# Kernel tuning notes

Measured on AMD Instinct MI355X. Metric: run time of the kernel, lower is better.

## Reference

```python
import jax, jax.numpy as jnp
import numpy as np
from jax import lax

B, TX, RX, RATE, DIMZ, HID, DIRS = 8192, 32, 32, 2, 64, 128, 2
S, FEAT = 2 * TX, 2 * TX + 1
BN_EPS = 1e-5
GD_STEP = 1e-6   # hardcoded in original forward
GD_ITERS = 10    # hardcoded in original forward


def setup_inputs() -> dict:
    key = jax.random.key(0)
    ks = jax.random.split(key, 9)
    sc = 1.0 / np.sqrt(HID)
    return {
        "y": jax.random.normal(ks[0], (B, 2 * RX), jnp.float32),
        "H": jax.random.normal(ks[1], (B, 2 * RX, 2 * TX), jnp.float32),
        "x_raw": jax.random.randint(ks[2], (B, 2 * TX, 1), 0, 2 ** RATE).astype(jnp.float32),
        "gru_w_ih": jax.random.uniform(ks[3], (DIRS, 3 * HID, FEAT), jnp.float32, -sc, sc),
        "gru_w_hh": jax.random.uniform(ks[4], (DIRS, 3 * HID, HID), jnp.float32, -sc, sc),
        "gru_b_ih": jax.random.uniform(ks[5], (DIRS, 3 * HID), jnp.float32, -sc, sc),
        "gru_b_hh": jax.random.uniform(ks[6], (DIRS, 3 * HID), jnp.float32, -sc, sc),
        "w_Wz": jax.random.normal(ks[7], (DIMZ, DIRS * HID), jnp.float32),
        "w_Wx": jax.random.normal(ks[8], (DIMZ, DIRS * HID), jnp.float32),
        "bn_gamma": jnp.ones((2 * TX,), jnp.float32),
        "bn_beta": jnp.zeros((2 * TX,), jnp.float32),
        "step_size": 1,
        "iterations": 10,
    }


def _gru_dir(x_seq, wih, whh, bih, bhh):
    # x_seq: (S, B, F); PyTorch GRU cell equations
    xg = jnp.einsum('sbf,gf->sbg', x_seq, wih) + bih  # (S, B, 3H)

    def step(h, xg_t):
        hg = h @ whh.T + bhh
        xr, xz, xn = jnp.split(xg_t, 3, axis=-1)
        hr, hz, hn = jnp.split(hg, 3, axis=-1)
        r = jax.nn.sigmoid(xr + hr)
        z = jax.nn.sigmoid(xz + hz)
        n = jnp.tanh(xn + r * hn)
        h = (1.0 - z) * n + z * h
        return h, h

    h0 = jnp.zeros((x_seq.shape[1], whh.shape[1]), x_seq.dtype)
    _, out = lax.scan(step, h0, xg)
    return out  # (S, B, H)


def reference(y, H, x_raw, gru_w_ih, gru_w_hh, gru_b_ih, gru_b_hh,
              w_Wz, w_Wx, bn_gamma, bn_beta, step_size, iterations):
    # Hty: (B, 2tx, 1), HtH: (B, 2tx, 2tx)
    Hty = jnp.einsum('brt,br->bt', H, y)[..., None]
    HtH = jnp.einsum('brt,bru->btu', H, H)

    # BatchNorm1d over channel dim 2tx (stats over batch and last dim)
    feats = jnp.concatenate([HtH, Hty], axis=-1)  # (B, 2tx, 2tx+1)
    mu = feats.mean(axis=(0, 2), keepdims=True)
    var = feats.var(axis=(0, 2), keepdims=True)
    feats = (feats - mu) / jnp.sqrt(var + BN_EPS)
    feats = feats * bn_gamma[None, :, None] + bn_beta[None, :, None]

    # bidirectional GRU over seq dim (seq_len = 2tx)
    x_seq = jnp.transpose(feats, (1, 0, 2))  # (S, B, F)
    fwd = _gru_dir(x_seq, gru_w_ih[0], gru_w_hh[0], gru_b_ih[0], gru_b_hh[0])
    bwd = _gru_dir(x_seq[::-1], gru_w_ih[1], gru_w_hh[1], gru_b_ih[1], gru_b_hh[1])[::-1]
    go = jnp.concatenate([fwd, bwd], axis=-1)  # (S, B, 2H)

    w_z = jnp.transpose(go @ w_Wz.T, (1, 2, 0))  # (B, dim_z, S)
    w_x = jnp.transpose(go @ w_Wx.T, (1, 0, 2))  # (B, S, dim_z)

    x_hat0 = 2.0 * x_raw - (2.0 ** RATE) + 1.0  # QAM symbols
    z0 = w_z @ x_hat0  # (B, dim_z, 1)

    # gradient-descent loop (step_size/iterations args ignored, as in source)
    wxt = jnp.swapaxes(w_x, 1, 2)        # (B, dim_z, 2tx)
    wxt_hty = wxt @ Hty                  # (B, dim_z, 1)
    whhw = wxt @ (HtH @ w_x)             # (B, dim_z, dim_z)
    two_step = 2.0 * GD_STEP

    def gd(zh, _):
        return zh + two_step * (wxt_hty - whhw @ zh), None

    z_hat, _ = lax.scan(gd, z0, None, length=GD_ITERS)
    return w_x @ z_hat  # (B, 2tx, 1)
```

## Files before the change

kernel.cpp:

```cpp
#include <hip/hip_runtime.h>
#include <math.h>


typedef __attribute__((ext_vector_type(8))) short s8v;
typedef __attribute__((ext_vector_type(4))) float f4v;

__device__ __forceinline__ short f2bf(float x) {
  unsigned u = __float_as_uint(x);
  u += 0x7fffu + ((u >> 16) & 1u);
  return (short)(u >> 16);
}
__device__ __forceinline__ float bf2f(short h) {
  return __uint_as_float(((unsigned)(unsigned short)h) << 16);
}
__device__ __forceinline__ void fma4(float4& c, float a, const float4 w) {
  c.x += a*w.x; c.y += a*w.y; c.z += a*w.z; c.w += a*w.w;
}
__device__ __forceinline__ float vget(const float4& v, int i) { return ((const float*)&v)[i]; }

#define MFMA(A, B, C) __builtin_amdgcn_mfma_f32_16x16x32_bf16((A), (B), (C), 0, 0, 0)

__global__ __launch_bounds__(256) void k_feats(
    const float* __restrict__ Hm, const float* __restrict__ y,
    short* __restrict__ fragX, float* __restrict__ htyU, float* __restrict__ bnacc)
{
  __shared__ __align__(16) float Hl[64][68];
  __shared__ float yl[64];
  __shared__ float s1[64], s2[64];
  const int b = blockIdx.x;
  const int tid = threadIdx.x;
  const float* Hb = Hm + (size_t)b*4096;
  for (int i = tid; i < 4096; i += 256) Hl[i>>6][i&63] = Hb[i];
  if (tid < 64) { yl[tid] = y[b*64+tid]; s1[tid] = 0.f; s2[tid] = 0.f; }
  __syncthreads();

  if (tid < 64) {
    float acc = 0.f;
    for (int r = 0; r < 64; ++r) acc += Hl[r][tid]*yl[r];
    htyU[tid*8192 + b] = acc;
    atomicAdd(&s1[tid], acc);
    atomicAdd(&s2[tid], acc*acc);
  }
  const int tg = tid & 15, ug = tid >> 4;
  float4 acc4[4];
  acc4[0]=acc4[1]=acc4[2]=acc4[3]=make_float4(0.f,0.f,0.f,0.f);
  for (int r = 0; r < 64; ++r) {
    const float4 tv = *(const float4*)&Hl[r][4*tg];
    const float4 uv = *(const float4*)&Hl[r][4*ug];
    #pragma unroll
    for (int tt=0;tt<4;++tt) fma4(acc4[tt], vget(tv,tt), uv);
  }
  const int mt   = (b >> 4) & 3;
  const int brow = b & 15;
  const int u0   = 4*ug;
  short* fbase = fragX + (size_t)(b >> 6)*64*8192
               + (mt*2 + (u0 >> 5))*512 + (brow + 16*((u0 >> 3) & 3))*8 + (u0 & 7);
  #pragma unroll
  for (int tt=0;tt<4;++tt) {
    const int t = 4*tg+tt;
    float sv=0.f, sq=0.f;
    short hib[4], lob[4];
    #pragma unroll
    for (int uu=0;uu<4;++uu) {
      const float v = vget(acc4[tt],uu);
      const short hi = f2bf(v);
      hib[uu] = hi; lob[uu] = f2bf(v - bf2f(hi));
      sv += v; sq += v*v;
    }
    short* dst = fbase + (size_t)t*8192;
    *(short4*)dst          = make_short4(hib[0],hib[1],hib[2],hib[3]);
    *(short4*)(dst + 4096) = make_short4(lob[0],lob[1],lob[2],lob[3]);
    sv += __shfl_down(sv,32); sq += __shfl_down(sq,32);
    sv += __shfl_down(sv,16); sq += __shfl_down(sq,16);
    if ((tid & 63) < 16) { atomicAdd(&s1[t], sv); atomicAdd(&s2[t], sq); }
  }
  __syncthreads();
  if (tid < 64) {
    atomicAdd(&bnacc[tid*16],      s1[tid]);
    atomicAdd(&bnacc[(64+tid)*16], s2[tid]);
  }
}

__global__ void k_bnfin(const float* __restrict__ bnacc, const float* __restrict__ gam,
                        const float* __restrict__ bet, float* __restrict__ bnac)
{
  const int t = threadIdx.x;
  if (t < 64) {
    const float inv = 1.f/532480.f;
    const float mu  = bnacc[t*16]*inv;
    const float var = bnacc[(64+t)*16]*inv - mu*mu;
    const float a = gam[t]*rsqrtf(var + 1e-5f);
    bnac[t] = a;
    bnac[64+t] = bet[t] - mu*a;
  }
}

__global__ __launch_bounds__(256) void k_prep(
    const float* __restrict__ wih, const float* __restrict__ whh,
    const float* __restrict__ Wz, const float* __restrict__ Wx,
    short* __restrict__ Wg, short* __restrict__ W2g, float* __restrict__ rowsum)
{
  const int i = blockIdx.x*256 + threadIdx.x;
  if (i < 294912) {
    const int dd = i / 147456, r = i % 147456;
    const int sp = r / 73728, r2 = r % 73728;
    const int chunk = r2 / 512, e = r2 % 512;
    const int lane = e >> 3, ii = e & 7;
    const int nt = chunk / 6, kt = chunk % 6;
    const int n = nt*16 + (lane & 15);
    const int k = kt*32 + (lane >> 4)*8 + ii;
    const float v = (k < 64) ? wih[dd*24960 + n*65 + k]
                             : whh[dd*49152 + n*128 + (k - 64)];
    const short hi = f2bf(v);
    Wg[i] = sp ? f2bf(v - bf2f(hi)) : hi;
  } else if (i < 360448) {
    const int t = i - 294912;
    const int dd = t / 32768, r = t % 32768;
    const int sp = r / 16384, r2 = r % 16384;
    const int chunk = r2 / 512, e = r2 % 512;
    const int lane = e >> 3, ii = e & 7;
    const int nt2 = chunk / 4, kt = chunk % 4;
    const int n2 = nt2*16 + (lane & 15);
    const int k = kt*32 + (lane >> 4)*8 + ii;
    const float v = (n2 < 64) ? Wx[n2*256 + dd*128 + k]
                              : Wz[(n2 - 64)*256 + dd*128 + k];
    const short hi = f2bf(v);
    W2g[t] = sp ? f2bf(v - bf2f(hi)) : hi;
  } else if (i < 361216) {
    const int t = i - 360448;
    const int dd = t / 384, g = t % 384;
    float ssum = 0.f;
    for (int f = 0; f < 65; ++f) ssum += wih[dd*24960 + g*65 + f];
    rowsum[t] = ssum;
  }
}

__global__ __launch_bounds__(512, 2) void k_scan(
    const short* __restrict__ fragX, const float* __restrict__ htyU,
    const float* __restrict__ xraw,
    const short* __restrict__ Wg, const short* __restrict__ W2g,
    const float* __restrict__ bih, const float* __restrict__ bhh,
    const float* __restrict__ rowsum, const float* __restrict__ bnac,
    const float* __restrict__ wih,
    float* __restrict__ wx_out, float* __restrict__ z0_out)
{
  __shared__ __align__(16) short Axb[16384];
  __shared__ __align__(16) short Ahb[32768];
  __shared__ __align__(16) float xl[64][68];
  __shared__ __align__(16) float htyl[64][68];
  __shared__ float bna[128];

  const int tid = threadIdx.x;
  const int l   = tid & 63;
  const int w   = __builtin_amdgcn_readfirstlane(tid >> 6);
  const int tile = blockIdx.x >> 1, d = blockIdx.x & 1;
  const int b0  = tile * 64;
  const int l15 = l & 15, lq = l >> 4;
  const int j   = 16*w + l15;

  const short* Wgd = Wg  + d*147456;
  const short* W2d = W2g + d*32768;
  float* wxo = wx_out + (size_t)d * (8192ull*4096ull);
  float* z0o = z0_out + (size_t)d * (8192ull*64ull);

  s8v BR[6][2], BZ[6][2], BN[6][2], BP[4][2];
  #pragma unroll
  for (int kt = 0; kt < 6; ++kt)
    #pragma unroll
    for (int sp = 0; sp < 2; ++sp) {
      BR[kt][sp] = *(const s8v*)&Wgd[((sp*24 + w     )*6 + kt)*512 + l*8];
      BZ[kt][sp] = *(const s8v*)&Wgd[((sp*24 + 8 + w )*6 + kt)*512 + l*8];
      BN[kt][sp] = *(const s8v*)&Wgd[((sp*24 + 16 + w)*6 + kt)*512 + l*8];
    }
  #pragma unroll
  for (int kt = 0; kt < 4; ++kt)
    #pragma unroll
    for (int sp = 0; sp < 2; ++sp)
      BP[kt][sp] = *(const s8v*)&W2d[((sp*8 + w)*4 + kt)*512 + l*8];

  const float rsR = rowsum[d*384 + j];
  const float rsZ = rowsum[d*384 + 128 + j];
  const float rsN = rowsum[d*384 + 256 + j];
  const float KR  = bih[d*384 + j]       + bhh[d*384 + j];
  const float KZ  = bih[d*384 + 128 + j] + bhh[d*384 + 128 + j];
  const float KN  = bih[d*384 + 256 + j];
  const float BHN = bhh[d*384 + 256 + j];
  const float w64r = wih[d*24960 + j*65 + 64];
  const float w64z = wih[d*24960 + (128 + j)*65 + 64];
  const float w64n = wih[d*24960 + (256 + j)*65 + 64];

  const int hw_base = (j >> 5)*512 + ((j >> 3) & 3)*128 + (j & 7);

  for (int i = tid; i < 32768; i += 512) Ahb[i] = 0;
  for (int i = tid; i < 4096; i += 512) {
    const int bl = i >> 6, s = i & 63;
    xl[s][bl] = 2.f*xraw[(size_t)(b0 + bl)*64 + s] - 3.f;
  }
  for (int i = tid; i < 4096; i += 512) {
    const int s = i >> 6, bl = i & 63;
    htyl[s][bl] = htyU[s*8192 + b0 + bl];
  }
  if (tid < 128) bna[tid] = bnac[tid];

  f4v hprev[4], z0a[4];
  #pragma unroll
  for (int mt = 0; mt < 4; ++mt) { hprev[mt] = (f4v)0.f; z0a[mt] = (f4v)0.f; }

  {
    const int s0 = d ? 63 : 0;
    const short* src = fragX + (size_t)(tile*64 + s0)*8192;
    *(float4*)((char*)Axb + tid*16)        = *(const float4*)((const char*)src + tid*16);
    *(float4*)((char*)Axb + 8192 + tid*16) = *(const float4*)((const char*)src + 8192 + tid*16);
  }
  __syncthreads();

  for (int it = 0; it < 64; ++it) {
    const int s  = d ? 63 - it : it;
    const int sn = (it < 63) ? (d ? s - 1 : s + 1) : s;

    short* AxR = Axb + ((it & 1) << 13);
    short* AxW = Axb + (((it + 1) & 1) << 13);
    short* AhR = Ahb + (((it + 1) & 1) << 14);
    short* AhW = Ahb + ((it & 1) << 14);

    const short* srcn = fragX + (size_t)(tile*64 + sn)*8192;
    const float4 pf0 = *(const float4*)((const char*)srcn + tid*16);
    const float4 pf1 = *(const float4*)((const char*)srcn + 8192 + tid*16);

    const float a_s = bna[s], c_s = bna[64 + s];
    const float crK = c_s*rsR + KR;
    const float czK = c_s*rsZ + KZ;
    const float cnK = c_s*rsN + KN;

    #pragma unroll
    for (int mt = 0; mt < 4; ++mt) {
      f4v Crx = (f4v)0.f, Czx = (f4v)0.f, Cnx = (f4v)0.f;
      f4v Crh = (f4v)0.f, Czh = (f4v)0.f, Cnh = (f4v)0.f;
      #pragma unroll
      for (int kt = 0; kt < 2; ++kt) {
        const s8v axh = *(const s8v*)&AxR[mt*1024 + kt*512 + l*8];
        const s8v axl = *(const s8v*)&AxR[4096 + mt*1024 + kt*512 + l*8];
        Crx = MFMA(axh, BR[kt][0], Crx); Crx = MFMA(axh, BR[kt][1], Crx); Crx = MFMA(axl, BR[kt][0], Crx);
        Czx = MFMA(axh, BZ[kt][0], Czx); Czx = MFMA(axh, BZ[kt][1], Czx); Czx = MFMA(axl, BZ[kt][0], Czx);
        Cnx = MFMA(axh, BN[kt][0], Cnx); Cnx = MFMA(axh, BN[kt][1], Cnx); Cnx = MFMA(axl, BN[kt][0], Cnx);
      }
      #pragma unroll
      for (int kh = 0; kh < 4; ++kh) {
        const s8v ahh = *(const s8v*)&AhR[mt*2048 + kh*512 + l*8];
        const s8v ahl = *(const s8v*)&AhR[8192 + mt*2048 + kh*512 + l*8];
        const int kt = 2 + kh;
        Crh = MFMA(ahh, BR[kt][0], Crh); Crh = MFMA(ahh, BR[kt][1], Crh); Crh = MFMA(ahl, BR[kt][0], Crh);
        Czh = MFMA(ahh, BZ[kt][0], Czh); Czh = MFMA(ahh, BZ[kt][1], Czh); Czh = MFMA(ahl, BZ[kt][0], Czh);
        Cnh = MFMA(ahh, BN[kt][0], Cnh); Cnh = MFMA(ahh, BN[kt][1], Cnh); Cnh = MFMA(ahl, BN[kt][0], Cnh);
      }
      const float4 av4 = *(const float4*)&htyl[s][mt*16 + lq*4];
      f4v av; av[0]=av4.x; av[1]=av4.y; av[2]=av4.z; av[3]=av4.w;
      Crx += av * w64r; Czx += av * w64z; Cnx += av * w64n;
      #pragma unroll
      for (int e = 0; e < 4; ++e) {
        const float rr  = 1.f/(1.f + __expf(-(a_s*Crx[e] + Crh[e] + crK)));
        const float zz  = 1.f/(1.f + __expf(-(a_s*Czx[e] + Czh[e] + czK)));
        const float pre = a_s*Cnx[e] + cnK + rr*(Cnh[e] + BHN);
        const float ax2 = fabsf(pre);
        const float ee  = __expf(-2.f*ax2);
        const float nn  = copysignf((1.f - ee)/(1.f + ee), pre);
        hprev[mt][e] = (1.f - zz)*nn + zz*hprev[mt][e];
      }
    }

    #pragma unroll
    for (int mt = 0; mt < 4; ++mt)
      #pragma unroll
      for (int e = 0; e < 4; ++e) {
        const float hv = hprev[mt][e];
        const short hi = f2bf(hv);
        const int ad = mt*2048 + hw_base + (lq*4 + e)*8;
        AhW[ad] = hi;
        AhW[8192 + ad] = f2bf(hv - bf2f(hi));
      }
    *(float4*)((char*)AxW + tid*16)        = pf0;
    *(float4*)((char*)AxW + 8192 + tid*16) = pf1;
    __syncthreads();

    #pragma unroll
    for (int mt = 0; mt < 4; ++mt) {
      f4v Cp = (f4v)0.f;
      #pragma unroll
      for (int kt = 0; kt < 4; ++kt) {
        const s8v ahh = *(const s8v*)&AhW[mt*2048 + kt*512 + l*8];
        const s8v ahl = *(const s8v*)&AhW[8192 + mt*2048 + kt*512 + l*8];
        Cp = MFMA(ahh, BP[kt][0], Cp);
        Cp = MFMA(ahh, BP[kt][1], Cp);
        Cp = MFMA(ahl, BP[kt][0], Cp);
      }
      if (w < 4) {
        #pragma unroll
        for (int e = 0; e < 4; ++e)
          wxo[(size_t)(b0 + mt*16 + lq*4 + e)*4096 + s*64 + 16*w + l15] = Cp[e];
      } else {
        const float4 xh4 = *(const float4*)&xl[s][mt*16 + lq*4];
        f4v xh; xh[0]=xh4.x; xh[1]=xh4.y; xh[2]=xh4.z; xh[3]=xh4.w;
        z0a[mt] += xh * Cp;
      }
    }
  }
  if (w >= 4) {
    #pragma unroll
    for (int mt = 0; mt < 4; ++mt)
      #pragma unroll
      for (int e = 0; e < 4; ++e)
        z0o[(size_t)(b0 + mt*16 + lq*4 + e)*64 + 16*(w-4) + l15] = z0a[mt][e];
  }
}

__global__ __launch_bounds__(256) void k_gd(
    const float* __restrict__ Hm, const float* __restrict__ y,
    const float* __restrict__ wxf, const float* __restrict__ wxb,
    const float* __restrict__ z0f, const float* __restrict__ z0b,
    float* __restrict__ out)
{
  __shared__ __align__(16) float Hl[64][68];
  __shared__ __align__(16) float wx[64][68];
  __shared__ __align__(16) float tmp[64][68];
  __shared__ float yl[64], wh[64], zv[64];
  const int b = blockIdx.x;
  const int tid = threadIdx.x;
  const float* Hb = Hm + (size_t)b*4096;
  for (int i = tid; i < 4096; i += 256) {
    Hl[i>>6][i&63] = Hb[i];
    wx[i>>6][i&63] = wxf[(size_t)b*4096 + i] + wxb[(size_t)b*4096 + i];
  }
  if (tid < 64) {
    yl[tid] = y[b*64+tid];
    zv[tid] = z0f[(size_t)b*64+tid] + z0b[(size_t)b*64+tid];
  }
  __syncthreads();
  const int zq = tid & 15, tq = tid >> 4;
  #pragma unroll
  for (int rr = 0; rr < 4; ++rr) {
    const int r = 4*tq + rr;
    float4 a = make_float4(0.f,0.f,0.f,0.f);
    for (int t = 0; t < 64; ++t) fma4(a, Hl[r][t], *(const float4*)&wx[t][4*zq]);
    *(float4*)&tmp[r][4*zq] = a;
  }
  __syncthreads();
  float (*ww)[68] = Hl;
  #pragma unroll
  for (int ii = 0; ii < 4; ++ii) {
    const int zi = 4*tq + ii;
    float4 a = make_float4(0.f,0.f,0.f,0.f);
    for (int r = 0; r < 64; ++r) fma4(a, tmp[r][zi], *(const float4*)&tmp[r][4*zq]);
    *(float4*)&ww[zi][4*zq] = a;
  }
  if (tid < 64) {
    float acc = 0.f;
    for (int r = 0; r < 64; ++r) acc += tmp[r][tid]*yl[r];
    wh[tid] = acc;
  }
  __syncthreads();
  for (int itr = 0; itr < 10; ++itr) {
    float nz = 0.f;
    if (tid < 64) {
      float mv = 0.f;
      for (int k2 = 0; k2 < 64; ++k2) mv += ww[tid][k2]*zv[k2];
      nz = zv[tid] + 2e-6f*(wh[tid] - mv);
    }
    __syncthreads();
    if (tid < 64) zv[tid] = nz;
    __syncthreads();
  }
  if (tid < 64) {
    float o = 0.f;
    for (int z2 = 0; z2 < 64; ++z2) o += wx[tid][z2]*zv[z2];
    out[(size_t)b*64 + tid] = o;
  }
}

extern "C" void kernel_launch(void* const* d_in, const int* in_sizes, int n_in,
                              void* d_out, int out_size, void* d_ws, size_t ws_size,
                              hipStream_t stream)
{
  const float* y    = (const float*)d_in[0];
  const float* Hm   = (const float*)d_in[1];
  const float* xraw = (const float*)d_in[2];
  const float* wih  = (const float*)d_in[3];
  const float* whh  = (const float*)d_in[4];
  const float* bih  = (const float*)d_in[5];
  const float* bhh  = (const float*)d_in[6];
  const float* Wz   = (const float*)d_in[7];
  const float* Wx   = (const float*)d_in[8];
  const float* gam  = (const float*)d_in[9];
  const float* bet  = (const float*)d_in[10];
  float* out = (float*)d_out;
  float* ws  = (float*)d_ws;

  float* wxf   = ws;
  float* wxb   = wxf + 33554432ull;
  float* z0f   = wxb + 33554432ull;
  float* z0b   = z0f + 524288ull;
  float* htyU  = z0b + 524288ull;
  float* rows  = htyU + 524288ull;
  float* bnacc = rows + 768ull;
  float* bnac  = bnacc + 2048ull;
  short* Wgs   = (short*)(bnac + 128ull);
  short* W2gs  = Wgs + 294912ull;
  short* fragX = W2gs + 65536ull;

  hipMemsetAsync(bnacc, 0, 2048*sizeof(float), stream);
  k_feats <<<8192, 256, 0, stream>>>(Hm, y, fragX, htyU, bnacc);
  k_prep  <<<1412, 256, 0, stream>>>(wih, whh, Wz, Wx, Wgs, W2gs, rows);
  k_bnfin <<<1, 64, 0, stream>>>(bnacc, gam, bet, bnac);
  k_scan  <<<256, 512, 0, stream>>>(fragX, htyU, xraw, Wgs, W2gs,
                                    bih, bhh, rows, bnac, wih, wxf, z0f);
  k_gd    <<<8192, 256, 0, stream>>>(Hm, y, wxf, wxb, z0f, z0b, out);
}
```

Measured before the change: 2.051 ms.

## Cut k_scan register pressure: async LDS prefetch, LDS constants and z0 accumulators

```diff
diff --git a/kernel.cpp b/kernel.cpp
--- a/kernel.cpp
+++ b/kernel.cpp
@@ -17,6 +17,12 @@
   c.x += a*w.x; c.y += a*w.y; c.z += a*w.z; c.w += a*w.w;
 }
 __device__ __forceinline__ float vget(const float4& v, int i) { return ((const float*)&v)[i]; }
+
+__device__ __forceinline__ void gload16(const void* g, void* l) {
+  __builtin_amdgcn_global_load_lds(
+      (const __attribute__((address_space(1))) void*)g,
+      (__attribute__((address_space(3))) void*)l, 16, 0, 0);
+}
 
 #define MFMA(A, B, C) __builtin_amdgcn_mfma_f32_16x16x32_bf16((A), (B), (C), 0, 0, 0)
 
@@ -147,7 +153,8 @@
   __shared__ __align__(16) short Axb[16384];
   __shared__ __align__(16) short Ahb[32768];
   __shared__ __align__(16) float xl[64][68];
-  __shared__ __align__(16) float htyl[64][68];
+  __shared__ __align__(16) float gcl[1536];
+  __shared__ __align__(16) float z0l[64][68];
   __shared__ float bna[128];
 
   const int tid = threadIdx.x;
@@ -157,6 +164,7 @@
   const int b0  = tile * 64;
   const int l15 = l & 15, lq = l >> 4;
   const int j   = 16*w + l15;
+  const int zcol = 16*(w & 3) + l15;
 
   const short* Wgd = Wg  + d*147456;
   const short* W2d = W2g + d*32768;
@@ -178,17 +186,6 @@
     for (int sp = 0; sp < 2; ++sp)
       BP[kt][sp] = *(const s8v*)&W2d[((sp*8 + w)*4 + kt)*512 + l*8];
 
-  const float rsR = rowsum[d*384 + j];
-  const float rsZ = rowsum[d*384 + 128 + j];
-  const float rsN = rowsum[d*384 + 256 + j];
-  const float KR  = bih[d*384 + j]       + bhh[d*384 + j];
-  const float KZ  = bih[d*384 + 128 + j] + bhh[d*384 + 128 + j];
-  const float KN  = bih[d*384 + 256 + j];
-  const float BHN = bhh[d*384 + 256 + j];
-  const float w64r = wih[d*24960 + j*65 + 64];
-  const float w64z = wih[d*24960 + (128 + j)*65 + 64];
-  const float w64n = wih[d*24960 + (256 + j)*65 + 64];
-
   const int hw_base = (j >> 5)*512 + ((j >> 3) & 3)*128 + (j & 7);
 
   for (int i = tid; i < 32768; i += 512) Ahb[i] = 0;
@@ -196,21 +193,34 @@
     const int bl = i >> 6, s = i & 63;
     xl[s][bl] = 2.f*xraw[(size_t)(b0 + bl)*64 + s] - 3.f;
   }
-  for (int i = tid; i < 4096; i += 512) {
-    const int s = i >> 6, bl = i & 63;
-    htyl[s][bl] = htyU[s*8192 + b0 + bl];
-  }
+  if (tid < 128) {
+    const int jj = tid;
+    float* g = &gcl[jj*12];
+    g[0] = rowsum[d*384 + jj];
+    g[1] = rowsum[d*384 + 128 + jj];
+    g[2] = rowsum[d*384 + 256 + jj];
+    g[3] = bih[d*384 + jj]       + bhh[d*384 + jj];
+    g[4] = bih[d*384 + 128 + jj] + bhh[d*384 + 128 + jj];
+    g[5] = bih[d*384 + 256 + jj];
+    g[6] = bhh[d*384 + 256 + jj];
+    g[7] = wih[d*24960 + jj*65 + 64];
+    g[8] = wih[d*24960 + (128 + jj)*65 + 64];
+    g[9] = wih[d*24960 + (256 + jj)*65 + 64];
+    g[10] = 0.f; g[11] = 0.f;
+  }
+  for (int i = tid; i < 64*68; i += 512) ((float*)z0l)[i] = 0.f;
   if (tid < 128) bna[tid] = bnac[tid];
 
-  f4v hprev[4], z0a[4];
-  #pragma unroll
-  for (int mt = 0; mt < 4; ++mt) { hprev[mt] = (f4v)0.f; z0a[mt] = (f4v)0.f; }
+  f4v hprev[4];
+  #pragma unroll
+  for (int mt = 0; mt < 4; ++mt) hprev[mt] = (f4v)0.f;
 
   {
     const int s0 = d ? 63 : 0;
-    const short* src = fragX + (size_t)(tile*64 + s0)*8192;
-    *(float4*)((char*)Axb + tid*16)        = *(const float4*)((const char*)src + tid*16);
-    *(float4*)((char*)Axb + 8192 + tid*16) = *(const float4*)((const char*)src + 8192 + tid*16);
+    const char* src0 = (const char*)(fragX + (size_t)(tile*64 + s0)*8192);
+    char* ax0 = (char*)Axb;
+    gload16(src0 + tid*16,        ax0 + w*1024);
+    gload16(src0 + 8192 + tid*16, ax0 + 8192 + w*1024);
   }
   __syncthreads();
 
@@ -218,22 +228,28 @@
     const int s  = d ? 63 - it : it;
     const int sn = (it < 63) ? (d ? s - 1 : s + 1) : s;
 
-    short* AxR = Axb + ((it & 1) << 13);
-    short* AxW = Axb + (((it + 1) & 1) << 13);
-    short* AhR = Ahb + (((it + 1) & 1) << 14);
-    short* AhW = Ahb + ((it & 1) << 14);
-
-    const short* srcn = fragX + (size_t)(tile*64 + sn)*8192;
-    const float4 pf0 = *(const float4*)((const char*)srcn + tid*16);
-    const float4 pf1 = *(const float4*)((const char*)srcn + 8192 + tid*16);
+    const short* AxR = Axb + ((it & 1) << 13);
+    char*        AxW = (char*)Axb + (((it + 1) & 1) << 14);
+    const short* AhR = Ahb + (((it + 1) & 1) << 14);
+    short*       AhW = Ahb + ((it & 1) << 14);
+
+    {
+      const char* srcn = (const char*)(fragX + (size_t)(tile*64 + sn)*8192);
+      gload16(srcn + tid*16,        AxW + w*1024);
+      gload16(srcn + 8192 + tid*16, AxW + 8192 + w*1024);
+    }
 
     const float a_s = bna[s], c_s = bna[64 + s];
-    const float crK = c_s*rsR + KR;
-    const float czK = c_s*rsZ + KZ;
-    const float cnK = c_s*rsN + KN;
+    const volatile float* gj = gcl + j*12;
+    const float crK  = c_s*gj[0] + gj[3];
+    const float czK  = c_s*gj[1] + gj[4];
+    const float cnK  = c_s*gj[2] + gj[5];
+    const float BHN  = gj[6];
+    const float w64r = gj[7], w64z = gj[8], w64n = gj[9];
 
     #pragma unroll
     for (int mt = 0; mt < 4; ++mt) {
+      const float4 av4 = *(const float4*)&htyU[s*8192 + b0 + mt*16 + lq*4];
       f4v Crx = (f4v)0.f, Czx = (f4v)0.f, Cnx = (f4v)0.f;
       f4v Crh = (f4v)0.f, Czh = (f4v)0.f, Cnh = (f4v)0.f;
       #pragma unroll
@@ -253,7 +269,6 @@
         Czh = MFMA(ahh, BZ[kt][0], Czh); Czh = MFMA(ahh, BZ[kt][1], Czh); Czh = MFMA(ahl, BZ[kt][0], Czh);
         Cnh = MFMA(ahh, BN[kt][0], Cnh); Cnh = MFMA(ahh, BN[kt][1], Cnh); Cnh = MFMA(ahl, BN[kt][0], Cnh);
       }
-      const float4 av4 = *(const float4*)&htyl[s][mt*16 + lq*4];
       f4v av; av[0]=av4.x; av[1]=av4.y; av[2]=av4.z; av[3]=av4.w;
       Crx += av * w64r; Czx += av * w64z; Cnx += av * w64n;
       #pragma unroll
@@ -278,8 +293,6 @@
         AhW[ad] = hi;
         AhW[8192 + ad] = f2bf(hv - bf2f(hi));
       }
-    *(float4*)((char*)AxW + tid*16)        = pf0;
-    *(float4*)((char*)AxW + 8192 + tid*16) = pf1;
     __syncthreads();
 
     #pragma unroll
@@ -298,9 +311,11 @@
         for (int e = 0; e < 4; ++e)
           wxo[(size_t)(b0 + mt*16 + lq*4 + e)*4096 + s*64 + 16*w + l15] = Cp[e];
       } else {
-        const float4 xh4 = *(const float4*)&xl[s][mt*16 + lq*4];
-        f4v xh; xh[0]=xh4.x; xh[1]=xh4.y; xh[2]=xh4.z; xh[3]=xh4.w;
-        z0a[mt] += xh * Cp;
+        #pragma unroll
+        for (int e = 0; e < 4; ++e) {
+          const int bl = mt*16 + lq*4 + e;
+          z0l[bl][zcol] += xl[s][bl] * Cp[e];
+        }
       }
     }
   }
@@ -308,8 +323,10 @@
     #pragma unroll
     for (int mt = 0; mt < 4; ++mt)
       #pragma unroll
-      for (int e = 0; e < 4; ++e)
-        z0o[(size_t)(b0 + mt*16 + lq*4 + e)*64 + 16*(w-4) + l15] = z0a[mt][e];
+      for (int e = 0; e < 4; ++e) {
+        const int bl = mt*16 + lq*4 + e;
+        z0o[(size_t)(b0 + bl)*64 + zcol] = z0l[bl][zcol];
+      }
   }
 }
 
```

Measured after the change: 2.167 ms. 1.06x slower.
